# Kernel tuning notes

Measured on AMD Instinct MI355X. Metric: run time of the kernel, lower is better.

The kernel has to match this reference:

```python
import jax, jax.numpy as jnp
import numpy as np

DIM = 384
HEADS = 6
HEAD_DIM = DIM // HEADS
HIDDEN = int(DIM * 4.0)
LS_INIT = 1e-5
EPS = 1e-5


def _ln(x, w, b):
    mu = jnp.mean(x, axis=-1, keepdims=True)
    var = jnp.var(x, axis=-1, keepdims=True)
    return (x - mu) * jax.lax.rsqrt(var + EPS) * w + b


def setup_inputs() -> dict:
    key = jax.random.key(0)
    ks = jax.random.split(key, 12)
    s = 0.02
    eye = jnp.eye(HIDDEN, dtype=jnp.float32)
    return {
        "x": jax.random.normal(ks[0], (8, 2048, DIM), dtype=jnp.float32),
        "qkv_w": jax.random.normal(ks[1], (3 * DIM, DIM), dtype=jnp.float32) * s,
        "qkv_b": jnp.zeros((3 * DIM,), dtype=jnp.float32),
        "proj_w": jax.random.normal(ks[2], (DIM, DIM), dtype=jnp.float32) * s,
        "proj_b": jnp.zeros((DIM,), dtype=jnp.float32),
        "fc1_w": jax.random.normal(ks[3], (HIDDEN, DIM), dtype=jnp.float32) * s,
        "fc1_b": jnp.zeros((HIDDEN,), dtype=jnp.float32),
        "eye1_w": eye + jax.random.normal(ks[4], (HIDDEN, HIDDEN), dtype=jnp.float32) * s,
        "eye2_w": eye + jax.random.normal(ks[5], (HIDDEN, HIDDEN), dtype=jnp.float32) * s,
        "fc2_w": jax.random.normal(ks[6], (DIM, HIDDEN), dtype=jnp.float32) * s,
        "fc2_b": jnp.zeros((DIM,), dtype=jnp.float32),
        "norm1_w": jnp.ones((DIM,), dtype=jnp.float32),
        "norm1_b": jnp.zeros((DIM,), dtype=jnp.float32),
        "norm2_w": jnp.ones((DIM,), dtype=jnp.float32),
        "norm2_b": jnp.zeros((DIM,), dtype=jnp.float32),
        "ls1_gamma": jnp.full((DIM,), LS_INIT, dtype=jnp.float32),
        "ls2_gamma": jnp.full((DIM,), LS_INIT, dtype=jnp.float32),
    }


def reference(x, qkv_w, qkv_b, proj_w, proj_b, fc1_w, fc1_b, eye1_w, eye2_w,
              fc2_w, fc2_b, norm1_w, norm1_b, norm2_w, norm2_b, ls1_gamma, ls2_gamma):
    B, N, C = x.shape
    scale = HEAD_DIM ** -0.5

    # ---- attention branch ----
    h = _ln(x, norm1_w, norm1_b)
    qkv = h @ qkv_w.T + qkv_b                      # [B,N,3C]
    qkv = qkv.reshape(B, N, 3, HEADS, HEAD_DIM)
    q = qkv[:, :, 0].transpose(0, 2, 1, 3) * scale  # [B,H,N,D]
    k = qkv[:, :, 1].transpose(0, 2, 1, 3)
    v = qkv[:, :, 2].transpose(0, 2, 1, 3)
    attn = jax.nn.softmax(jnp.einsum('bhnd,bhmd->bhnm', q, k), axis=-1)  # [B,H,N,N]
    o = jnp.einsum('bhnm,bhmd->bhnd', attn, v)
    o = o.transpose(0, 2, 1, 3).reshape(B, N, C)
    o = o @ proj_w.T + proj_b
    x = x + o * ls1_gamma

    # ---- extended MLP branch (timm Mlp norm is Identity) ----
    h2 = _ln(x, norm2_w, norm2_b)
    a = jax.nn.gelu(h2 @ fc1_w.T + fc1_b, approximate=False)
    a = (a @ eye1_w.T) @ eye2_w.T
    a = a @ fc2_w.T + fc2_b
    return x + a * ls2_gamma
```

## Files before the change

### kernel.cpp

```cpp
#include <hip/hip_runtime.h>
#include <math.h>

#define DIM 384
#define HEADS 6
#define HEAD_DIM 64
#define HIDDEN 1536
#define BATCH 8
#define SEQ 2048
#define TOKENS (BATCH * SEQ)

typedef __bf16 bf16;
typedef float f32x4 __attribute__((ext_vector_type(4)));
typedef float f32x16 __attribute__((ext_vector_type(16)));
typedef int i32x2 __attribute__((ext_vector_type(2)));
typedef int i32x4 __attribute__((ext_vector_type(4)));
typedef int i32x8 __attribute__((ext_vector_type(8)));

#define GLOAD_LDS(gp, lp)                                                      \
    __builtin_amdgcn_global_load_lds(                                          \
        (const __attribute__((address_space(1))) void*)(gp),                   \
        (__attribute__((address_space(3))) void*)(lp), 16, 0, 0)

__device__ __forceinline__ unsigned char to_fp8(float v) {
    return (unsigned char)(__builtin_amdgcn_cvt_pk_fp8_f32(v, v, 0, false) & 0xff);
}

__device__ __forceinline__ i32x8 pack8(i32x4 lo, i32x4 hi) {
    i32x8 r;
#pragma unroll
    for (int j = 0; j < 4; j++) { r[j] = lo[j]; r[4 + j] = hi[j]; }
    return r;
}

#define NW_QKV  (1152 * 384)
#define NW_PROJ (384 * 384)
#define NW_FC1  (1536 * 384)
#define NW_EYE  (1536 * 1536)
#define NW_FC2  (384 * 1536)
#define NW_ALL2 (NW_QKV + NW_PROJ + NW_FC1 + NW_EYE + NW_FC2)

template <int EPI>
__device__ __forceinline__ void gemm_core(const unsigned char* __restrict__ A,
                                          const unsigned char* __restrict__ W,
                                          const float* __restrict__ bias,
                                          float* __restrict__ outf,
                                          const float* __restrict__ resid,
                                          const float* __restrict__ gamma,
                                          unsigned char* __restrict__ vtb8,
                                          unsigned char* __restrict__ out8,
                                          int N, int K, int bx, int by,
                                          unsigned char* As, unsigned char* Bs) {
    int tid = threadIdx.x;
    int wave = tid >> 6, lane = tid & 63;
    int l15 = lane & 15, quad = lane >> 4;
    int bm = by * 128, bn = bx * 128;
    int wm = (wave & 1) * 64, wn = (wave >> 1) * 64;
    f32x4 acc[4][4] = {};

    for (int k0 = 0; k0 < K; k0 += 128) {
#pragma unroll
        for (int i = 0; i < 4; i++) {
            int slot = i * 256 + tid;
            int rr = slot >> 3;
            int gg = (slot & 7) ^ (rr & 7);
            GLOAD_LDS(A + (size_t)(bm + rr) * K + k0 + gg * 16,
                      (char*)As + (i * 256 + wave * 64) * 16);
            GLOAD_LDS(W + (size_t)(bn + rr) * K + k0 + gg * 16,
                      (char*)Bs + (i * 256 + wave * 64) * 16);
        }
        __syncthreads();
        i32x8 af[4], bfr[4];
#pragma unroll
        for (int mt = 0; mt < 4; mt++) {
            int rA = wm + mt * 16 + l15;
            const i32x4* p = (const i32x4*)(As + 128 * rA);
            af[mt] = pack8(p[(2 * quad) ^ (rA & 7)], p[(2 * quad + 1) ^ (rA & 7)]);
        }
#pragma unroll
        for (int nt = 0; nt < 4; nt++) {
            int rB = wn + nt * 16 + l15;
            const i32x4* p = (const i32x4*)(Bs + 128 * rB);
            bfr[nt] = pack8(p[(2 * quad) ^ (rB & 7)], p[(2 * quad + 1) ^ (rB & 7)]);
        }
#pragma unroll
        for (int mt = 0; mt < 4; mt++)
#pragma unroll
            for (int nt = 0; nt < 4; nt++)
                acc[mt][nt] = __builtin_amdgcn_mfma_scale_f32_16x16x128_f8f6f4(
                    af[mt], bfr[nt], acc[mt][nt], 0, 0,
                    0, 0x7f7f7f7f, 0, 0x7f7f7f7f);
        __syncthreads();
    }

#pragma unroll
    for (int mt = 0; mt < 4; mt++) {
#pragma unroll
        for (int nt = 0; nt < 4; nt++) {
            int col = bn + wn + nt * 16 + l15;
            int row0 = bm + wm + mt * 16 + quad * 4;
            float v[4];
#pragma unroll
            for (int r = 0; r < 4; r++) {
                v[r] = acc[mt][nt][r];
                if (EPI >= 2) v[r] += bias[col];
                if (EPI == 2) v[r] = 0.5f * v[r] * (1.f + erff(v[r] * 0.70710678118654752f));
            }
            if (EPI == 3) {
#pragma unroll
                for (int r = 0; r < 4; r++) {
                    size_t idx = (size_t)(row0 + r) * N + col;
                    outf[idx] = resid[idx] + v[r] * gamma[col];
                }
            } else if (EPI == 4) {
                if (col < 768) {
                    float sc = (col < 384) ? 0.180336880f : 1.f;
#pragma unroll
                    for (int r = 0; r < 4; r++)
                        out8[(size_t)(row0 + r) * 768 + col] = to_fp8(v[r] * sc);
                } else {
                    int hd = col - 768;
                    int b = row0 >> 11;
                    int n0 = row0 & 2047;
                    int p = __builtin_amdgcn_cvt_pk_fp8_f32(v[0], v[1], 0, false);
                    p = __builtin_amdgcn_cvt_pk_fp8_f32(v[2], v[3], p, true);
                    *(int*)(vtb8 + ((size_t)(b * 384 + hd) << 11) + n0) = p;
                }
            } else {
#pragma unroll
                for (int r = 0; r < 4; r++)
                    out8[(size_t)(row0 + r) * N + col] = to_fp8(v[r]);
            }
        }
    }
}

template <int EPI>
__global__ __launch_bounds__(256) void gemm_f8(const unsigned char* __restrict__ A,
                                               const unsigned char* __restrict__ W,
                                               const float* __restrict__ bias,
                                               float* __restrict__ outf,
                                               const float* __restrict__ resid,
                                               const float* __restrict__ gamma,
                                               unsigned char* __restrict__ vtb8,
                                               unsigned char* __restrict__ out8,
                                               int N, int K) {
    __shared__ __attribute__((aligned(16))) unsigned char As[128 * 128];
    __shared__ __attribute__((aligned(16))) unsigned char Bs[128 * 128];
    gemm_core<EPI>(A, W, bias, outf, resid, gamma, vtb8, out8, N, K,
                   blockIdx.x, blockIdx.y, As, Bs);
}

__global__ __launch_bounds__(256) void fused_pre(const float* __restrict__ x,
                                                 const float* __restrict__ n1w,
                                                 const float* __restrict__ n1b,
                                                 unsigned char* __restrict__ hbuf8,
                                                 const float* __restrict__ e1,
                                                 unsigned char* __restrict__ e1t8,
                                                 const float* __restrict__ qkv,
                                                 const float* __restrict__ proj,
                                                 const float* __restrict__ fc1,
                                                 const float* __restrict__ e2,
                                                 const float* __restrict__ fc2,
                                                 unsigned char* __restrict__ w8) {
    __shared__ float tb[64][65];
    int bid = blockIdx.x;
    int tid = threadIdx.x;
    if (bid < 4096) {
        int wave = tid >> 6, lane = tid & 63;
        int tok = bid * 4 + wave;
        const float* xr = x + (size_t)tok * DIM;
        float v[6];
        float s = 0.f;
#pragma unroll
        for (int i = 0; i < 6; i++) { v[i] = xr[lane + 64 * i]; s += v[i]; }
#pragma unroll
        for (int m = 1; m < 64; m <<= 1) s += __shfl_xor(s, m, 64);
        float mu = s * (1.f / DIM);
        float q = 0.f;
#pragma unroll
        for (int i = 0; i < 6; i++) { float d = v[i] - mu; q += d * d; }
#pragma unroll
        for (int m = 1; m < 64; m <<= 1) q += __shfl_xor(q, m, 64);
        float rstd = rsqrtf(q * (1.f / DIM) + 1e-5f);
        unsigned char* orow = hbuf8 + (size_t)tok * DIM;
#pragma unroll
        for (int i = 0; i < 6; i++) {
            int c = lane + 64 * i;
            orow[c] = to_fp8((v[i] - mu) * rstd * n1w[c] + n1b[c]);
        }
    } else if (bid < 4096 + 576) {
        int g = bid - 4096;
        int r0 = (g / 24) * 64, c0 = (g % 24) * 64;
        int tc = tid & 63, tr = tid >> 6;
#pragma unroll
        for (int i = 0; i < 16; i++) {
            int r = tr + 4 * i;
            tb[r][tc] = e1[(size_t)(r0 + r) * 1536 + c0 + tc];
        }
        __syncthreads();
        int on = tid >> 2;
        int ok0 = (tid & 3) * 16;
        i32x4 pk;
#pragma unroll
        for (int q = 0; q < 4; q++) {
            int p = __builtin_amdgcn_cvt_pk_fp8_f32(tb[ok0 + 4 * q + 0][on],
                                                    tb[ok0 + 4 * q + 1][on], 0, false);
            p = __builtin_amdgcn_cvt_pk_fp8_f32(tb[ok0 + 4 * q + 2][on],
                                                tb[ok0 + 4 * q + 3][on], p, true);
            pk[q] = p;
        }
        *(i32x4*)(e1t8 + (size_t)(c0 + on) * 1536 + r0 + ok0) = pk;
    } else {
        int q4 = (bid - 4672) * 256 + tid;
        for (; q4 < NW_ALL2 / 4; q4 += 1024 * 256) {
            int i = q4 * 4;
            int j = i;
            const float* src;
            if (j < NW_QKV) src = qkv;
            else if ((j -= NW_QKV) < NW_PROJ) src = proj;
            else if ((j -= NW_PROJ) < NW_FC1) src = fc1;
            else if ((j -= NW_FC1) < NW_EYE) src = e2;
            else { j -= NW_EYE; src = fc2; }
            float4 v = *(const float4*)(src + j);
            int p = __builtin_amdgcn_cvt_pk_fp8_f32(v.x, v.y, 0, false);
            p = __builtin_amdgcn_cvt_pk_fp8_f32(v.z, v.w, p, true);
            *(int*)(w8 + i) = p;
        }
    }
}

__global__ __launch_bounds__(256) void gemm_qkv_prep(const unsigned char* __restrict__ hbuf8,
                                                     const unsigned char* __restrict__ wqkv8,
                                                     const float* __restrict__ qkv_b,
                                                     unsigned char* __restrict__ vtb8,
                                                     unsigned char* __restrict__ qk8,
                                                     const unsigned char* __restrict__ e1t8,
                                                     const unsigned char* __restrict__ weye28,
                                                     unsigned char* __restrict__ m1t8) {
    __shared__ __attribute__((aligned(16))) unsigned char As[128 * 128];
    __shared__ __attribute__((aligned(16))) unsigned char Bs[128 * 128];
    int bid = blockIdx.x;
    if (bid < 144) {
        gemm_core<0>(e1t8, weye28, nullptr, nullptr, nullptr, nullptr, nullptr, m1t8,
                     1536, 1536, bid % 12, bid / 12, As, Bs);
    } else {
        int g = bid - 144;
        gemm_core<4>(hbuf8, wqkv8, qkv_b, nullptr, nullptr, nullptr, vtb8, qk8,
                     1152, 384, g % 9, g / 9, As, Bs);
    }
}

__global__ __launch_bounds__(256) void gemm_fc1_prep(const unsigned char* __restrict__ hbuf8,
                                                     const unsigned char* __restrict__ wfc18,
                                                     const float* __restrict__ fc1_b,
                                                     unsigned char* __restrict__ abuf8,
                                                     const unsigned char* __restrict__ wfc28,
                                                     const unsigned char* __restrict__ m1t8,
                                                     unsigned char* __restrict__ wc8) {
    __shared__ __attribute__((aligned(16))) unsigned char As[128 * 128];
    __shared__ __attribute__((aligned(16))) unsigned char Bs[128 * 128];
    int bid = blockIdx.x;
    if (bid < 36) {
        gemm_core<0>(wfc28, m1t8, nullptr, nullptr, nullptr, nullptr, nullptr, wc8,
                     1536, 1536, bid % 12, bid / 12, As, Bs);
    } else {
        int g = bid - 36;
        gemm_core<2>(hbuf8, wfc18, fc1_b, nullptr, nullptr, nullptr, nullptr, abuf8,
                     1536, 384, g % 12, g / 12, As, Bs);
    }
}

__global__ __launch_bounds__(256) void gemm_projln(const unsigned char* __restrict__ A,
                                                   const unsigned char* __restrict__ W,
                                                   const float* __restrict__ bias,
                                                   const float* __restrict__ resid,
                                                   const float* __restrict__ gamma,
                                                   const float* __restrict__ n2w,
                                                   const float* __restrict__ n2b,
                                                   float* __restrict__ x1,
                                                   unsigned char* __restrict__ hbuf8) {
    __shared__ __attribute__((aligned(16))) unsigned char As[64 * 128];
    __shared__ __attribute__((aligned(16))) unsigned char Bs[384 * 128];
    int tid = threadIdx.x;
    int wave = tid >> 6, lane = tid & 63;
    int l15 = lane & 15, quad = lane >> 4;
    int bm = blockIdx.x * 64;
    int wm = wave * 16;
    f32x4 acc[24];
#pragma unroll
    for (int i = 0; i < 24; i++) acc[i] = (f32x4){0.f, 0.f, 0.f, 0.f};

    const int K = 384;
    for (int k0 = 0; k0 < K; k0 += 128) {
#pragma unroll
        for (int i = 0; i < 2; i++) {
            int slot = i * 256 + tid;
            int rr = slot >> 3, gg = (slot & 7) ^ (rr & 7);
            GLOAD_LDS(A + (size_t)(bm + rr) * K + k0 + gg * 16, (char*)As + slot * 16);
        }
#pragma unroll
        for (int i = 0; i < 12; i++) {
            int slot = i * 256 + tid;
            int rr = slot >> 3, gg = (slot & 7) ^ (rr & 7);
            GLOAD_LDS(W + (size_t)rr * K + k0 + gg * 16, (char*)Bs + slot * 16);
        }
        __syncthreads();
        int rA = wm + l15;
        const i32x4* pa = (const i32x4*)(As + 128 * rA);
        i32x8 af = pack8(pa[(2 * quad) ^ (rA & 7)], pa[(2 * quad + 1) ^ (rA & 7)]);
#pragma unroll
        for (int nt = 0; nt < 24; nt++) {
            int rB = nt * 16 + l15;
            const i32x4* pb = (const i32x4*)(Bs + 128 * rB);
            i32x8 bf = pack8(pb[(2 * quad) ^ (rB & 7)], pb[(2 * quad + 1) ^ (rB & 7)]);
            acc[nt] = __builtin_amdgcn_mfma_scale_f32_16x16x128_f8f6f4(
                af, bf, acc[nt], 0, 0, 0, 0x7f7f7f7f, 0, 0x7f7f7f7f);
        }
        __syncthreads();
    }

    int row0 = bm + wm + quad * 4;
#pragma unroll
    for (int nt = 0; nt < 24; nt++) {
        int col = nt * 16 + l15;
        float bi = bias[col], ga = gamma[col];
#pragma unroll
        for (int r = 0; r < 4; r++) {
            size_t idx = (size_t)(row0 + r) * DIM + col;
            float v = resid[idx] + (acc[nt][r] + bi) * ga;
            x1[idx] = v;
            acc[nt][r] = v;
        }
    }
#pragma unroll
    for (int r = 0; r < 4; r++) {
        float s = 0.f;
#pragma unroll
        for (int nt = 0; nt < 24; nt++) s += acc[nt][r];
#pragma unroll
        for (int m = 1; m < 16; m <<= 1) s += __shfl_xor(s, m, 64);
        float mu = s * (1.f / DIM);
        float q = 0.f;
#pragma unroll
        for (int nt = 0; nt < 24; nt++) { float d = acc[nt][r] - mu; q += d * d; }
#pragma unroll
        for (int m = 1; m < 16; m <<= 1) q += __shfl_xor(q, m, 64);
        float rstd = rsqrtf(q * (1.f / DIM) + 1e-5f);
        unsigned char* orow = hbuf8 + (size_t)(row0 + r) * DIM;
#pragma unroll
        for (int nt = 0; nt < 24; nt++) {
            int col = nt * 16 + l15;
            orow[col] = to_fp8((acc[nt][r] - mu) * rstd * n2w[col] + n2b[col]);
        }
    }
}

__global__ __launch_bounds__(256, 3) void attn_kernel(const unsigned char* __restrict__ qk8,
                                                      const unsigned char* __restrict__ vtb8,
                                                      unsigned char* __restrict__ o) {
    __shared__ __attribute__((aligned(16))) unsigned char Ks[2][128 * 64];
    __shared__ __attribute__((aligned(16))) unsigned char Vts[2][64 * 128];
    int tid = threadIdx.x, wave = tid >> 6, lane = tid & 63;
    int l31 = lane & 31, h = lane >> 5;
    int bh = blockIdx.y;
    int b = bh / HEADS, hh = bh - b * HEADS;
    int qr0 = blockIdx.x * 128 + wave * 32;
    const unsigned char* base = qk8 + (size_t)b * SEQ * 768;
    const unsigned char* vbase = vtb8 + ((size_t)bh << 17);

    int kr0 = tid >> 2, kr1 = (tid + 256) >> 2, ks = tid & 3;
    const unsigned char* kg0 = base + (size_t)kr0 * 768 + 384 + hh * 64 + 16 * (ks ^ ((kr0 >> 1) & 3));
    const unsigned char* kg1 = base + (size_t)kr1 * 768 + 384 + hh * 64 + 16 * (ks ^ ((kr1 >> 1) & 3));
    int vr0 = tid >> 3, vr1 = (tid + 256) >> 3, vs = tid & 7;
    const unsigned char* vg0 = vbase + ((size_t)vr0 << 11) + 16 * (vs ^ ((vr0 >> 1) & 3));
    const unsigned char* vg1 = vbase + ((size_t)vr1 << 11) + 16 * (vs ^ ((vr1 >> 1) & 3));
    int lo0 = tid * 16, lo1 = (tid + 256) * 16;

    i32x8 aq = *(const i32x8*)(base + (size_t)(qr0 + l31) * 768 + hh * 64 + 32 * h);

    f32x16 oa0 = {}, oa1 = {};
    float lsum = 0.f;
    int swr = (l31 >> 1) & 3;

    GLOAD_LDS(kg0, (char*)Ks[0] + lo0);
    GLOAD_LDS(kg1, (char*)Ks[0] + lo1);
    GLOAD_LDS(vg0, (char*)Vts[0] + lo0);
    GLOAD_LDS(vg1, (char*)Vts[0] + lo1);
    __syncthreads();

    for (int kt = 0; kt < SEQ / 128; kt++) {
        const unsigned char* Kc = Ks[kt & 1];
        const unsigned char* Vc = Vts[kt & 1];
        if (kt + 1 < SEQ / 128) {
            char* kn = (char*)Ks[(kt + 1) & 1];
            char* vn = (char*)Vts[(kt + 1) & 1];
            size_t kadv = (size_t)(kt + 1) * 128 * 768;
            int vadv = (kt + 1) * 128;
            GLOAD_LDS(kg0 + kadv, kn + lo0);
            GLOAD_LDS(kg1 + kadv, kn + lo1);
            GLOAD_LDS(vg0 + vadv, vn + lo0);
            GLOAD_LDS(vg1 + vadv, vn + lo1);
        }

        int pk[4][4];
#pragma unroll
        for (int mi = 0; mi < 4; mi++) {
            int rK = 32 * mi + l31;
            const i32x4* kp = (const i32x4*)(Kc + rK * 64);
            i32x8 ak = pack8(kp[(2 * h + 0) ^ swr], kp[(2 * h + 1) ^ swr]);
            f32x16 s = {};
            s = __builtin_amdgcn_mfma_scale_f32_32x32x64_f8f6f4(
                ak, aq, s, 0, 0, 0, 0x7f7f7f7f, 0, 0x7f7f7f7f);
#pragma unroll
            for (int g = 0; g < 4; g++) {
                float p0 = __builtin_amdgcn_exp2f(s[4 * g + 0]);
                float p1 = __builtin_amdgcn_exp2f(s[4 * g + 1]);
                float p2 = __builtin_amdgcn_exp2f(s[4 * g + 2]);
                float p3 = __builtin_amdgcn_exp2f(s[4 * g + 3]);
                lsum += (p0 + p1) + (p2 + p3);
                int pkv = __builtin_amdgcn_cvt_pk_fp8_f32(p0, p1, 0, false);
                pkv = __builtin_amdgcn_cvt_pk_fp8_f32(p2, p3, pkv, true);
                pk[mi][g] = pkv;
            }
        }

        i32x8 ap0, ap1;
#pragma unroll
        for (int g = 0; g < 4; g++) {
            i32x2 r0 = __builtin_amdgcn_permlane32_swap(pk[0][g], pk[1][g], false, false);
            ap0[2 * g] = r0[0];
            ap0[2 * g + 1] = r0[1];
            i32x2 r1 = __builtin_amdgcn_permlane32_swap(pk[2][g], pk[3][g], false, false);
            ap1[2 * g] = r1[0];
            ap1[2 * g + 1] = r1[1];
        }

        {
            const i32x4* vp0 = (const i32x4*)(Vc + l31 * 128);
            const i32x4* vp1 = (const i32x4*)(Vc + (32 + l31) * 128);
            i32x8 bv00 = pack8(vp0[(2 * h + 0) ^ swr], vp0[(2 * h + 1) ^ swr]);
            i32x8 bv01 = pack8(vp0[4 + ((2 * h + 0) ^ swr)], vp0[4 + ((2 * h + 1) ^ swr)]);
            i32x8 bv10 = pack8(vp1[(2 * h + 0) ^ swr], vp1[(2 * h + 1) ^ swr]);
            i32x8 bv11 = pack8(vp1[4 + ((2 * h + 0) ^ swr)], vp1[4 + ((2 * h + 1) ^ swr)]);
            oa0 = __builtin_amdgcn_mfma_scale_f32_32x32x64_f8f6f4(
                ap0, bv00, oa0, 0, 0, 0, 0x7f7f7f7f, 0, 0x7f7f7f7f);
            oa0 = __builtin_amdgcn_mfma_scale_f32_32x32x64_f8f6f4(
                ap1, bv01, oa0, 0, 0, 0, 0x7f7f7f7f, 0, 0x7f7f7f7f);
            oa1 = __builtin_amdgcn_mfma_scale_f32_32x32x64_f8f6f4(
                ap0, bv10, oa1, 0, 0, 0, 0x7f7f7f7f, 0, 0x7f7f7f7f);
            oa1 = __builtin_amdgcn_mfma_scale_f32_32x32x64_f8f6f4(
                ap1, bv11, oa1, 0, 0, 0, 0x7f7f7f7f, 0, 0x7f7f7f7f);
        }
        __syncthreads();
    }

    lsum += __shfl_xor(lsum, 32, 64);

#pragma unroll
    for (int g = 0; g < 4; g++) {
#pragma unroll
        for (int r4 = 0; r4 < 4; r4++) {
            int qloc = r4 + 8 * g + 4 * h;
            float inv = 1.f / __shfl(lsum, qloc, 64);
            int r = 4 * g + r4;
            unsigned char* orow = o + ((size_t)(b * SEQ + qr0 + qloc)) * DIM + hh * 64;
            orow[l31]      = to_fp8(oa0[r] * inv);
            orow[32 + l31] = to_fp8(oa1[r] * inv);
        }
    }
}

extern "C" void kernel_launch(void* const* d_in, const int* in_sizes, int n_in,
                              void* d_out, int out_size, void* d_ws, size_t ws_size,
                              hipStream_t stream) {
    const float* x      = (const float*)d_in[0];
    const float* qkv_w  = (const float*)d_in[1];
    const float* qkv_b  = (const float*)d_in[2];
    const float* proj_w = (const float*)d_in[3];
    const float* proj_b = (const float*)d_in[4];
    const float* fc1_w  = (const float*)d_in[5];
    const float* fc1_b  = (const float*)d_in[6];
    const float* eye1_w = (const float*)d_in[7];
    const float* eye2_w = (const float*)d_in[8];
    const float* fc2_w  = (const float*)d_in[9];
    const float* fc2_b  = (const float*)d_in[10];
    const float* n1w    = (const float*)d_in[11];
    const float* n1b    = (const float*)d_in[12];
    const float* n2w    = (const float*)d_in[13];
    const float* n2b    = (const float*)d_in[14];
    const float* ls1    = (const float*)d_in[15];
    const float* ls2    = (const float*)d_in[16];
    float* out = (float*)d_out;

    char* w = (char*)d_ws;
    size_t off = 0;
    unsigned char* w8 = (unsigned char*)(w + off); off += (size_t)NW_ALL2;
    unsigned char* wqkv8  = w8;
    unsigned char* wproj8 = wqkv8 + NW_QKV;
    unsigned char* wfc18  = wproj8 + NW_PROJ;
    unsigned char* weye28 = wfc18 + NW_FC1;
    unsigned char* wfc28  = weye28 + NW_EYE;
    unsigned char* e1t8  = (unsigned char*)(w + off); off += (size_t)NW_EYE;
    unsigned char* m1t8  = (unsigned char*)(w + off); off += (size_t)NW_EYE;
    unsigned char* wc8   = (unsigned char*)(w + off); off += (size_t)NW_FC2;
    unsigned char* hbuf8 = (unsigned char*)(w + off); off += (size_t)TOKENS * DIM;
    unsigned char* qk8   = (unsigned char*)(w + off); off += (size_t)TOKENS * 768;
    unsigned char* vtb8  = (unsigned char*)(w + off); off += (size_t)TOKENS * DIM;
    unsigned char* obuf8 = (unsigned char*)(w + off); off += (size_t)TOKENS * DIM;
    unsigned char* abuf8 = (unsigned char*)(w + off); off += (size_t)TOKENS * HIDDEN;
    float* x1   = (float*)(w + off); off += (size_t)TOKENS * DIM * 4;

    fused_pre<<<5696, 256, 0, stream>>>(x, n1w, n1b, hbuf8, eye1_w, e1t8,
                                        qkv_w, proj_w, fc1_w, eye2_w, fc2_w, w8);

    gemm_qkv_prep<<<144 + 1152, 256, 0, stream>>>(hbuf8, wqkv8, qkv_b, vtb8, qk8,
                                                  e1t8, weye28, m1t8);

    attn_kernel<<<dim3(SEQ / 128, BATCH * HEADS), 256, 0, stream>>>(qk8, vtb8, obuf8);

    gemm_projln<<<TOKENS / 64, 256, 0, stream>>>(obuf8, wproj8, proj_b, x, ls1,
                                                 n2w, n2b, x1, hbuf8);

    gemm_fc1_prep<<<36 + 1536, 256, 0, stream>>>(hbuf8, wfc18, fc1_b, abuf8,
                                                 wfc28, m1t8, wc8);

    gemm_f8<3><<<dim3(384 / 128, TOKENS / 128), 256, 0, stream>>>(
        abuf8, wc8, fc2_b, out, x1, ls2, nullptr, nullptr, 384, 1536);
}
```

Baseline: 301.6 us.

## Reassociate weight-chain folding to avoid the large eye1·eye2 GEMM

Weight folding is reassociated so the combined fc2·eye2·eye1 matrix is built as (fc2·eye2)·eye1, two 384x1536x1536 GEMMs instead of a 1536x1536x1536 GEMM followed by a smaller one. eye2 is now transposed to fp8 alongside eye1 in the prep kernel. The second fold GEMM is moved into the proj+LN kernel launch so it runs concurrently with that stage. fc1 now runs as its own launch instead of being bundled with fold work. The intent is to cut weight-fold FLOPs and shorten the critical path, at the cost of an extra fp8 rounding step in the fold and a different fp8 quantization order.

```diff
diff --git a/kernel.cpp b/kernel.cpp
--- a/kernel.cpp
+++ b/kernel.cpp
@@ -37,7 +37,7 @@
 #define NW_FC1  (1536 * 384)
 #define NW_EYE  (1536 * 1536)
 #define NW_FC2  (384 * 1536)
-#define NW_ALL2 (NW_QKV + NW_PROJ + NW_FC1 + NW_EYE + NW_FC2)
+#define NW_ALL3 (NW_QKV + NW_PROJ + NW_FC1 + NW_FC2)
 
 template <int EPI>
 __device__ __forceinline__ void gemm_core(const unsigned char* __restrict__ A,
@@ -156,10 +156,11 @@
                                                  unsigned char* __restrict__ hbuf8,
                                                  const float* __restrict__ e1,
                                                  unsigned char* __restrict__ e1t8,
+                                                 const float* __restrict__ e2,
+                                                 unsigned char* __restrict__ e2t8,
                                                  const float* __restrict__ qkv,
                                                  const float* __restrict__ proj,
                                                  const float* __restrict__ fc1,
-                                                 const float* __restrict__ e2,
                                                  const float* __restrict__ fc2,
                                                  unsigned char* __restrict__ w8) {
     __shared__ float tb[64][65];
@@ -188,14 +189,17 @@
             int c = lane + 64 * i;
             orow[c] = to_fp8((v[i] - mu) * rstd * n1w[c] + n1b[c]);
         }
-    } else if (bid < 4096 + 576) {
+    } else if (bid < 5248) {
         int g = bid - 4096;
+        const float* src = e1;
+        unsigned char* dst = e1t8;
+        if (g >= 576) { g -= 576; src = e2; dst = e2t8; }
         int r0 = (g / 24) * 64, c0 = (g % 24) * 64;
         int tc = tid & 63, tr = tid >> 6;
 #pragma unroll
         for (int i = 0; i < 16; i++) {
             int r = tr + 4 * i;
-            tb[r][tc] = e1[(size_t)(r0 + r) * 1536 + c0 + tc];
+            tb[r][tc] = src[(size_t)(r0 + r) * 1536 + c0 + tc];
         }
         __syncthreads();
         int on = tid >> 2;
@@ -209,23 +213,20 @@
                                                 tb[ok0 + 4 * q + 3][on], p, true);
             pk[q] = p;
         }
-        *(i32x4*)(e1t8 + (size_t)(c0 + on) * 1536 + r0 + ok0) = pk;
+        *(i32x4*)(dst + (size_t)(c0 + on) * 1536 + r0 + ok0) = pk;
     } else {
-        int q4 = (bid - 4672) * 256 + tid;
-        for (; q4 < NW_ALL2 / 4; q4 += 1024 * 256) {
-            int i = q4 * 4;
-            int j = i;
-            const float* src;
-            if (j < NW_QKV) src = qkv;
-            else if ((j -= NW_QKV) < NW_PROJ) src = proj;
-            else if ((j -= NW_PROJ) < NW_FC1) src = fc1;
-            else if ((j -= NW_FC1) < NW_EYE) src = e2;
-            else { j -= NW_EYE; src = fc2; }
-            float4 v = *(const float4*)(src + j);
-            int p = __builtin_amdgcn_cvt_pk_fp8_f32(v.x, v.y, 0, false);
-            p = __builtin_amdgcn_cvt_pk_fp8_f32(v.z, v.w, p, true);
-            *(int*)(w8 + i) = p;
-        }
+        int q4 = (bid - 5248) * 256 + tid;
+        int i = q4 * 4;
+        int j = i;
+        const float* src;
+        if (j < NW_QKV) src = qkv;
+        else if ((j -= NW_QKV) < NW_PROJ) src = proj;
+        else if ((j -= NW_PROJ) < NW_FC1) src = fc1;
+        else { j -= NW_FC1; src = fc2; }
+        float4 v = *(const float4*)(src + j);
+        int p = __builtin_amdgcn_cvt_pk_fp8_f32(v.x, v.y, 0, false);
+        p = __builtin_amdgcn_cvt_pk_fp8_f32(v.z, v.w, p, true);
+        *(int*)(w8 + i) = p;
     }
 }
 
@@ -234,57 +235,36 @@
                                                      const float* __restrict__ qkv_b,
                                                      unsigned char* __restrict__ vtb8,
                                                      unsigned char* __restrict__ qk8,
-                                                     const unsigned char* __restrict__ e1t8,
-                                                     const unsigned char* __restrict__ weye28,
-                                                     unsigned char* __restrict__ m1t8) {
-    __shared__ __attribute__((aligned(16))) unsigned char As[128 * 128];
-    __shared__ __attribute__((aligned(16))) unsigned char Bs[128 * 128];
-    int bid = blockIdx.x;
-    if (bid < 144) {
-        gemm_core<0>(e1t8, weye28, nullptr, nullptr, nullptr, nullptr, nullptr, m1t8,
-                     1536, 1536, bid % 12, bid / 12, As, Bs);
-    } else {
-        int g = bid - 144;
-        gemm_core<4>(hbuf8, wqkv8, qkv_b, nullptr, nullptr, nullptr, vtb8, qk8,
-                     1152, 384, g % 9, g / 9, As, Bs);
-    }
-}
-
-__global__ __launch_bounds__(256) void gemm_fc1_prep(const unsigned char* __restrict__ hbuf8,
-                                                     const unsigned char* __restrict__ wfc18,
-                                                     const float* __restrict__ fc1_b,
-                                                     unsigned char* __restrict__ abuf8,
                                                      const unsigned char* __restrict__ wfc28,
-                                                     const unsigned char* __restrict__ m1t8,
-                                                     unsigned char* __restrict__ wc8) {
+                                                     const unsigned char* __restrict__ e2t8,
+                                                     unsigned char* __restrict__ wfe8) {
     __shared__ __attribute__((aligned(16))) unsigned char As[128 * 128];
     __shared__ __attribute__((aligned(16))) unsigned char Bs[128 * 128];
     int bid = blockIdx.x;
     if (bid < 36) {
-        gemm_core<0>(wfc28, m1t8, nullptr, nullptr, nullptr, nullptr, nullptr, wc8,
+        gemm_core<0>(wfc28, e2t8, nullptr, nullptr, nullptr, nullptr, nullptr, wfe8,
                      1536, 1536, bid % 12, bid / 12, As, Bs);
     } else {
         int g = bid - 36;
-        gemm_core<2>(hbuf8, wfc18, fc1_b, nullptr, nullptr, nullptr, nullptr, abuf8,
-                     1536, 384, g % 12, g / 12, As, Bs);
-    }
-}
-
-__global__ __launch_bounds__(256) void gemm_projln(const unsigned char* __restrict__ A,
-                                                   const unsigned char* __restrict__ W,
-                                                   const float* __restrict__ bias,
-                                                   const float* __restrict__ resid,
-                                                   const float* __restrict__ gamma,
-                                                   const float* __restrict__ n2w,
-                                                   const float* __restrict__ n2b,
-                                                   float* __restrict__ x1,
-                                                   unsigned char* __restrict__ hbuf8) {
-    __shared__ __attribute__((aligned(16))) unsigned char As[64 * 128];
-    __shared__ __attribute__((aligned(16))) unsigned char Bs[384 * 128];
+        gemm_core<4>(hbuf8, wqkv8, qkv_b, nullptr, nullptr, nullptr, vtb8, qk8,
+                     1152, 384, g % 9, g / 9, As, Bs);
+    }
+}
+
+__device__ __forceinline__ void projln_core(const unsigned char* __restrict__ A,
+                                            const unsigned char* __restrict__ W,
+                                            const float* __restrict__ bias,
+                                            const float* __restrict__ resid,
+                                            const float* __restrict__ gamma,
+                                            const float* __restrict__ n2w,
+                                            const float* __restrict__ n2b,
+                                            float* __restrict__ x1,
+                                            unsigned char* __restrict__ hbuf8,
+                                            int bidx, unsigned char* As, unsigned char* Bs) {
     int tid = threadIdx.x;
     int wave = tid >> 6, lane = tid & 63;
     int l15 = lane & 15, quad = lane >> 4;
-    int bm = blockIdx.x * 64;
+    int bm = bidx * 64;
     int wm = wave * 16;
     f32x4 acc[24];
 #pragma unroll
@@ -352,6 +332,29 @@
             int col = nt * 16 + l15;
             orow[col] = to_fp8((acc[nt][r] - mu) * rstd * n2w[col] + n2b[col]);
         }
+    }
+}
+
+__global__ __launch_bounds__(256) void gemm_projln_prep(const unsigned char* __restrict__ obuf8,
+                                                        const unsigned char* __restrict__ wproj8,
+                                                        const float* __restrict__ proj_b,
+                                                        const float* __restrict__ x,
+                                                        const float* __restrict__ ls1,
+                                                        const float* __restrict__ n2w,
+                                                        const float* __restrict__ n2b,
+                                                        float* __restrict__ x1,
+                                                        unsigned char* __restrict__ hbuf8,
+                                                        const unsigned char* __restrict__ wfe8,
+                                                        const unsigned char* __restrict__ e1t8,
+                                                        unsigned char* __restrict__ wc8) {
+    __shared__ __attribute__((aligned(16))) unsigned char smem[448 * 128];
+    int bid = blockIdx.x;
+    if (bid < 36) {
+        gemm_core<0>(wfe8, e1t8, nullptr, nullptr, nullptr, nullptr, nullptr, wc8,
+                     1536, 1536, bid % 12, bid / 12, smem, smem + 128 * 128);
+    } else {
+        projln_core(obuf8, wproj8, proj_b, x, ls1, n2w, n2b, x1, hbuf8,
+                    bid - 36, smem, smem + 64 * 128);
     }
 }
 
@@ -494,14 +497,14 @@
 
     char* w = (char*)d_ws;
     size_t off = 0;
-    unsigned char* w8 = (unsigned char*)(w + off); off += (size_t)NW_ALL2;
+    unsigned char* w8 = (unsigned char*)(w + off); off += (size_t)NW_ALL3;
     unsigned char* wqkv8  = w8;
     unsigned char* wproj8 = wqkv8 + NW_QKV;
     unsigned char* wfc18  = wproj8 + NW_PROJ;
-    unsigned char* weye28 = wfc18 + NW_FC1;
-    unsigned char* wfc28  = weye28 + NW_EYE;
+    unsigned char* wfc28  = wfc18 + NW_FC1;
     unsigned char* e1t8  = (unsigned char*)(w + off); off += (size_t)NW_EYE;
-    unsigned char* m1t8  = (unsigned char*)(w + off); off += (size_t)NW_EYE;
+    unsigned char* e2t8  = (unsigned char*)(w + off); off += (size_t)NW_EYE;
+    unsigned char* wfe8  = (unsigned char*)(w + off); off += (size_t)NW_FC2;
     unsigned char* wc8   = (unsigned char*)(w + off); off += (size_t)NW_FC2;
     unsigned char* hbuf8 = (unsigned char*)(w + off); off += (size_t)TOKENS * DIM;
     unsigned char* qk8   = (unsigned char*)(w + off); off += (size_t)TOKENS * 768;
@@ -510,19 +513,21 @@
     unsigned char* abuf8 = (unsigned char*)(w + off); off += (size_t)TOKENS * HIDDEN;
     float* x1   = (float*)(w + off); off += (size_t)TOKENS * DIM * 4;
 
-    fused_pre<<<5696, 256, 0, stream>>>(x, n1w, n1b, hbuf8, eye1_w, e1t8,
-                                        qkv_w, proj_w, fc1_w, eye2_w, fc2_w, w8);
-
-    gemm_qkv_prep<<<144 + 1152, 256, 0, stream>>>(hbuf8, wqkv8, qkv_b, vtb8, qk8,
-                                                  e1t8, weye28, m1t8);
+    fused_pre<<<4096 + 1152 + 1728, 256, 0, stream>>>(
+        x, n1w, n1b, hbuf8, eye1_w, e1t8, eye2_w, e2t8,
+        qkv_w, proj_w, fc1_w, fc2_w, w8);
+
+    gemm_qkv_prep<<<36 + 1152, 256, 0, stream>>>(hbuf8, wqkv8, qkv_b, vtb8, qk8,
+                                                 wfc28, e2t8, wfe8);
 
     attn_kernel<<<dim3(SEQ / 128, BATCH * HEADS), 256, 0, stream>>>(qk8, vtb8, obuf8);
 
-    gemm_projln<<<TOKENS / 64, 256, 0, stream>>>(obuf8, wproj8, proj_b, x, ls1,
-                                                 n2w, n2b, x1, hbuf8);
-
-    gemm_fc1_prep<<<36 + 1536, 256, 0, stream>>>(hbuf8, wfc18, fc1_b, abuf8,
-                                                 wfc28, m1t8, wc8);
+    gemm_projln_prep<<<36 + 256, 256, 0, stream>>>(obuf8, wproj8, proj_b, x, ls1,
+                                                   n2w, n2b, x1, hbuf8,
+                                                   wfe8, e1t8, wc8);
+
+    gemm_f8<2><<<dim3(1536 / 128, TOKENS / 128), 256, 0, stream>>>(
+        hbuf8, wfc18, fc1_b, nullptr, nullptr, nullptr, nullptr, abuf8, 1536, 384);
 
     gemm_f8<3><<<dim3(384 / 128, TOKENS / 128), 256, 0, stream>>>(
         abuf8, wc8, fc2_b, out, x1, ls2, nullptr, nullptr, 384, 1536);
```

Measured after the change: 276.5 us. 1.09x faster.
